# Performance work log

Measured on AMD Instinct MI355X. Metric: run time of the kernel, lower is better.

Reference implementation:

```python
import jax, jax.numpy as jnp
from jax import lax
import numpy as np

K = 256   # kernel_size == hidden channels (Haar basis size)
S = 16    # stride
BN_EPS = 1e-5


def _haar_matrix_unnorm(n):
    if n == 2:
        return np.array([[1.0, 1.0], [1.0, -1.0]])
    prev = _haar_matrix_unnorm(n // 2)
    top = np.kron(prev, np.array([1.0, 1.0]))
    bot = np.kron(np.eye(n // 2), np.array([1.0, -1.0]))
    return np.concatenate((top, bot))


def haar_matrix(n):
    h = _haar_matrix_unnorm(n)
    return h / np.linalg.norm(h, axis=1, keepdims=True)


def setup_inputs() -> dict:
    key = jax.random.key(0)
    ks = jax.random.split(key, 8)
    B, T = 64, 32768
    haar = jnp.asarray(haar_matrix(K), dtype=jnp.float32)          # [K, K]
    x = jax.random.normal(ks[0], (B, 1, T), dtype=jnp.float32)
    return {
        "x": x,
        # BitwiseConv1d(1, K, K, stride=S, padding=K)
        "conv_w": haar[:, None, :],                                 # [K, 1, K] (OIH)
        "conv_b": 0.01 * jax.random.normal(ks[1], (K,), dtype=jnp.float32),
        "conv_gate": jax.random.uniform(ks[2], (K, 1, K), dtype=jnp.float32),
        "conv_scale": jnp.ones((K,), dtype=jnp.float32),            # adaptive per-out-channel scale
        # BatchNorm1d(K)
        "bn_gamma": jnp.ones((K,), dtype=jnp.float32),
        "bn_beta": jnp.zeros((K,), dtype=jnp.float32),
        # BitwiseConvTranspose1d(K, 1, K, stride=S)
        "ct_w": haar.T[:, None, :],                                 # [K(in), 1(out), K] (IOH, torch layout)
        "ct_b": 0.01 * jax.random.normal(ks[3], (1,), dtype=jnp.float32),
        "ct_gate": jax.random.uniform(ks[4], (K, 1, K), dtype=jnp.float32),
        "ct_scale": jnp.ones((1,), dtype=jnp.float32),
    }


def _forward(x, conv_w, conv_b, conv_gate, conv_scale, bn_gamma, bn_beta,
             ct_w, ct_b, ct_gate, ct_scale):
    T = x.shape[2]
    # --- BitwiseConv1d: gated weights (in_bin/weight_bin = identity) ---
    # gate binarization maps gate -> (gate + 1) / 2, multiplied into weights
    w = conv_w * (conv_gate + 1.0) * 0.5                            # [K,1,K]
    h = lax.conv_general_dilated(
        x, w, window_strides=(S,), padding=[(K, K)],
        dimension_numbers=("NCH", "OIH", "NCH"))                  # [B,K,L]
    h = conv_scale[None, :, None] * (h + conv_b[None, :, None])    # adaptive scaling
    # --- ReLU then BatchNorm1d (training-mode batch statistics) ---
    h = jax.nn.relu(h)
    mu = jnp.mean(h, axis=(0, 2), keepdims=True)
    var = jnp.mean((h - mu) ** 2, axis=(0, 2), keepdims=True)
    h = (h - mu) * lax.rsqrt(var + BN_EPS)
    h = h * bn_gamma[None, :, None] + bn_beta[None, :, None]
    # --- BitwiseConvTranspose1d: gated weights, expressed as dilated conv ---
    wt = ct_w * (ct_gate + 1.0) * 0.5                               # [K_in, 1, K]
    # torch IOH -> regular-conv OIH with kernel flipped
    wr = jnp.flip(jnp.transpose(wt, (1, 0, 2)), axis=-1)            # [1, K, K]
    y = lax.conv_general_dilated(
        h, wr, window_strides=(1,), padding=[(K - 1, K - 1)],
        lhs_dilation=(S,), dimension_numbers=("NCH", "OIH", "NCH"))
    y = ct_scale[None, :, None] * (y + ct_b[None, :, None])
    # crop: out[:, :, K : T + K]
    return y[:, :, K:T + K]


def reference(x, conv_w, conv_b, conv_gate, conv_scale, bn_gamma, bn_beta,
              ct_w, ct_b, ct_gate, ct_scale):
    return _forward(x, conv_w, conv_b, conv_gate, conv_scale, bn_gamma, bn_beta,
                    ct_w, ct_b, ct_gate, ct_scale)
```

## Files before the change

kernel.cpp:

```cpp
#include <hip/hip_runtime.h>
#include <hip/hip_bf16.h>

#define BB 64
#define TT 32768
#define KK 256
#define LL 2065
#define NLT 9
#define NPART (BB*NLT)
#define NJ 19
#define HBSTR 72
#define NPT3 16
#define XG 2336

typedef __attribute__((ext_vector_type(8))) short short8;
typedef __attribute__((ext_vector_type(4))) float f32x4;
typedef __attribute__((ext_vector_type(4))) int int4v;
typedef __attribute__((ext_vector_type(2))) unsigned int uint2v;

__device__ __forceinline__ unsigned short f2bf(float f) {
    unsigned u = __builtin_bit_cast(unsigned, f);
    unsigned r = (u + 0x7FFFu + ((u >> 16) & 1u)) >> 16;
    return (unsigned short)r;
}
__device__ __forceinline__ unsigned pkbf(float a, float b) {
    unsigned r;
    asm("v_cvt_pk_bf16_f32 %0, %1, %2" : "=v"(r) : "v"(a), "v"(b));
    return r;
}
__device__ __forceinline__ void gload_lds16(const void* g, void* l) {
    __builtin_amdgcn_global_load_lds(
        (const __attribute__((address_space(1))) unsigned int*)g,
        (__attribute__((address_space(3))) unsigned int*)l, 16, 0, 0);
}

__global__ void k0x_xbf(const float* __restrict__ x, unsigned short* __restrict__ xbf)
{
    int idx = blockIdx.x*256 + threadIdx.x;
    int b = idx / XG, gi = idx - b*XG;
    unsigned short* dst = xbf + (size_t)idx*24;
    int4v w0, w1;
    if (gi < 16 || gi > 2063) {
        w0 = (int4v){0,0,0,0}; w1 = (int4v){0,0,0,0};
    } else {
        const float4* xv = (const float4*)(x + (size_t)b*TT + 16*(gi-16));
        float4 a0 = xv[0], a1 = xv[1], a2 = xv[2], a3 = xv[3];
        w0 = (int4v){ (int)pkbf(a0.x,a0.y), (int)pkbf(a0.z,a0.w),
                      (int)pkbf(a1.x,a1.y), (int)pkbf(a1.z,a1.w) };
        w1 = (int4v){ (int)pkbf(a2.x,a2.y), (int)pkbf(a2.z,a2.w),
                      (int)pkbf(a3.x,a3.y), (int)pkbf(a3.z,a3.w) };
    }
    *(int4v*)dst       = w0;
    *(int4v*)(dst + 8) = w1;
}

__global__ void k0_w1f(const float* __restrict__ cw, const float* __restrict__ cgt,
                       const float* __restrict__ cs, const float* __restrict__ cb,
                       unsigned short* __restrict__ W1f, float* __restrict__ cbs)
{
    int idx = blockIdx.x*256 + threadIdx.x;
    int lane = idx & 63, ntL = (idx>>6)&7, kk = (idx>>9)&7, half = idx>>12;
    int o = half*128 + ntL*16 + (lane&15);
    float sc = cs[o];
    int kbase = kk*32 + ((lane>>4)<<3);
    short8 v;
    #pragma unroll
    for (int i = 0; i < 8; ++i) {
        int gi = o*KK + kbase + i;
        v[i] = (short)f2bf(sc * cw[gi]*(cgt[gi]+1.0f)*0.5f);
    }
    *(short8*)(W1f + (size_t)idx*8) = v;
    if (blockIdx.x == 0) {
        int c = threadIdx.x;
        cbs[c] = cs[c]*cb[c];
    }
}

__global__ __launch_bounds__(256, 3)
void k1_conv(const unsigned short* __restrict__ xbf, const float* __restrict__ cbs,
             const unsigned short* __restrict__ W1f,
             unsigned short* __restrict__ hout,
             float* __restrict__ psum, float* __restrict__ psq)
{
    __shared__ __align__(16) char smem[13312 + 32768];
    char* xwinb = smem;
    char* wbuf  = smem + 13312;
    unsigned short* hb = (unsigned short*)smem;
    float* redS = (float*)(smem + 36864);
    float* redQ = (float*)(smem + 36864 + 4096);

    const int tid   = threadIdx.x;
    const int q     = blockIdx.x & 3;
    const int ltile = blockIdx.x >> 2;
    const int b     = blockIdx.y;
    const int l0    = ltile * 256;
    const int lane  = tid & 63;
    const int w     = tid >> 6;

    {
        #pragma unroll
        for (int it = 0; it < 8; ++it) {
            int ci = w*8 + it;
            int kk = ci >> 2, ntl = ci & 3;
            size_t so = (size_t)((((q>>1)*8 + kk)*8 + (q&1)*4 + ntl))*1024;
            gload_lds16((const char*)W1f + so + lane*16, wbuf + ci*1024);
        }
    }
    {
        const char* xsrc = (const char*)xbf + (size_t)b*(XG*48) + (size_t)ltile*12288;
        #pragma unroll
        for (int it = 0; it < 4; ++it) {
            int i = w + it*4;
            if (i < 13)
                gload_lds16(xsrc + i*1024 + lane*16, xwinb + i*1024);
        }
    }
    __syncthreads();

    f32x4 acc[4][4];
    #pragma unroll
    for (int mt = 0; mt < 4; ++mt)
        #pragma unroll
        for (int nt = 0; nt < 4; ++nt) acc[mt][nt] = (f32x4){0.f,0.f,0.f,0.f};

    const int gq = lane >> 4;
    const int Gt = 16*gq + 16*(gq>>1);
    const int abase = 48*((w<<6) + (lane & 15)) + Gt;

    #pragma unroll
    for (int kk = 0; kk < 8; ++kk) {
        short8 bfx[4], afw[4];
        #pragma unroll
        for (int nt = 0; nt < 4; ++nt)
            bfx[nt] = *(const short8*)(xwinb + abase + nt*768 + kk*96);
        #pragma unroll
        for (int mt = 0; mt < 4; ++mt)
            afw[mt] = *(const short8*)(wbuf + (kk*4 + mt)*1024 + lane*16);
        __builtin_amdgcn_s_setprio(1);
        #pragma unroll
        for (int mt = 0; mt < 4; ++mt)
            #pragma unroll
            for (int nt = 0; nt < 4; ++nt)
                acc[mt][nt] = __builtin_amdgcn_mfma_f32_16x16x32_bf16(afw[mt], bfx[nt], acc[mt][nt], 0, 0, 0);
        __builtin_amdgcn_s_setprio(0);
    }
    __syncthreads();

    const int c0 = q*64;
    const int g  = lane >> 4;
    const int li = lane & 15;
    #pragma unroll
    for (int mt = 0; mt < 4; ++mt) {
        int cq = c0 + mt*16 + g*4;
        f32x4 cbs4 = *(const f32x4*)&cbs[cq];
        f32x4 s4 = (f32x4){0.f,0.f,0.f,0.f};
        f32x4 q4 = (f32x4){0.f,0.f,0.f,0.f};
        #pragma unroll
        for (int nt = 0; nt < 4; ++nt) {
            int lloc = (w<<6) + nt*16 + li;
            f32x4 hv;
            #pragma unroll
            for (int rr = 0; rr < 4; ++rr)
                hv[rr] = fmaxf(acc[mt][nt][rr] + cbs4[rr], 0.0f);
            uint2v pkv = { pkbf(hv[0], hv[1]), pkbf(hv[2], hv[3]) };
            *(uint2v*)(hb + lloc*HBSTR + mt*16 + g*4) = pkv;
            if (l0 + lloc < LL) { s4 += hv; q4 += hv*hv; }
        }
        #pragma unroll
        for (int d = 1; d < 4; d <<= 1) {
            #pragma unroll
            for (int rr = 0; rr < 4; ++rr) {
                s4[rr] += __shfl_xor(s4[rr], d);
                q4[rr] += __shfl_xor(q4[rr], d);
            }
        }
        if ((li & 3) == 0) {
            int slot = ((w*4 + mt)*4 + g)*4 + (li >> 2);
            *(f32x4*)&redS[slot*4] = s4;
            *(f32x4*)&redQ[slot*4] = q4;
        }
    }
    __syncthreads();

    {
        const int rsub = tid >> 3;
        const int cpos = tid & 7;
        #pragma unroll
        for (int it = 0; it < 8; ++it) {
            int row = it*32 + rsub;
            int l = l0 + row;
            if (l < LL) {
                int4v v = *(const int4v*)(hb + row*HBSTR + cpos*8);
                *(int4v*)(hout + (((size_t)(b*LL + l)) << 8) + q*64 + cpos*8) = v;
            }
        }
    }
    if (tid < 64) {
        int mt = tid >> 4, gg = (tid >> 2) & 3, rr = tid & 3;
        float s = 0.f, qq = 0.f;
        #pragma unroll
        for (int wv = 0; wv < 4; ++wv)
            #pragma unroll
            for (int l4 = 0; l4 < 4; ++l4) {
                int slot = ((wv*4 + mt)*4 + gg)*4 + l4;
                s  += redS[slot*4 + rr];
                qq += redQ[slot*4 + rr];
            }
        int c = c0 + tid;
        int slot = b*NLT + ltile;
        psum[c*NPART + slot] = s;
        psq [c*NPART + slot] = qq;
    }
}

__global__ __launch_bounds__(256)
void k2_bn(const float* __restrict__ psum, const float* __restrict__ psq,
           const float* __restrict__ bng, const float* __restrict__ bnb,
           const float* __restrict__ ctw, const float* __restrict__ ctg,
           const float* __restrict__ ctscale,
           float* __restrict__ W3s, float* __restrict__ SWS)
{
    __shared__ double rs[4], rq[4];
    __shared__ float s_a, s_bc;
    __shared__ float swl[256];
    const int c = blockIdx.x;
    const int tid = threadIdx.x;
    double s = 0.0, q = 0.0;
    for (int i = tid; i < NPART; i += 256) {
        s += (double)psum[c*NPART + i];
        q += (double)psq [c*NPART + i];
    }
    for (int off = 32; off > 0; off >>= 1) {
        s += __shfl_down(s, off);
        q += __shfl_down(q, off);
    }
    if ((tid & 63) == 0) { rs[tid >> 6] = s; rq[tid >> 6] = q; }
    __syncthreads();
    if (tid == 0) {
        double st = rs[0]+rs[1]+rs[2]+rs[3];
        double qt = rq[0]+rq[1]+rq[2]+rq[3];
        const double cnt = (double)BB * (double)LL;
        double mu = st / cnt;
        double var = qt / cnt - mu*mu;
        float rsig = (float)(1.0 / sqrt(var + 1e-5));
        float a = bng[c] * rsig;
        s_a = a;
        s_bc = bnb[c] - (float)mu * a;
    }
    __syncthreads();
    float a = s_a, bc = s_bc, scl = ctscale[0];
    int gi = c*KK + tid;
    float wt = ctw[gi] * (ctg[gi] + 1.0f) * 0.5f;
    W3s[tid*KK + c] = scl * a * wt;
    swl[tid] = wt * bc;
    __syncthreads();
    if (tid < 16) {
        float acc2 = 0.0f;
        #pragma unroll
        for (int d = 0; d < 16; ++d) acc2 += swl[d*16 + tid];
        SWS[c*16 + tid] = acc2;
    }
}

__global__ __launch_bounds__(256)
void k2b_const(const float* __restrict__ SWS, const float* __restrict__ ctb,
               const float* __restrict__ ctscale, float* __restrict__ C2)
{
    __shared__ float accb[16][17];
    int tid = threadIdx.x;
    int r = tid & 15, cc = tid >> 4;
    float s = 0.0f;
    #pragma unroll
    for (int i = 0; i < 16; ++i) s += SWS[(cc*16 + i)*16 + r];
    accb[cc][r] = s;
    __syncthreads();
    if (tid < 16) {
        float t = 0.0f;
        #pragma unroll
        for (int i = 0; i < 16; ++i) t += accb[i][tid];
        C2[tid] = ctscale[0] * (t + ctb[0]);
    }
}

__global__ void k2c_b2f(const float* __restrict__ W3s, unsigned short* __restrict__ B2f)
{
    int idx = blockIdx.x*256 + threadIdx.x;
    int lane = idx & 63;
    int ntG  = (idx>>6) & 3;
    int kk   = (idx>>8) & 7;
    int j    = idx>>11;
    int c    = kk*32 + ((lane>>4)<<3);
    int r    = lane & 15;
    int d    = ntG + 15 - j;
    short8 v;
    if (d >= 0 && d <= 15) {
        const float* wr = W3s + (size_t)(16*d + r)*KK + c;
        #pragma unroll
        for (int i = 0; i < 8; ++i) v[i] = (short)f2bf(wr[i]);
    } else {
        #pragma unroll
        for (int i = 0; i < 8; ++i) v[i] = 0;
    }
    *(short8*)(B2f + (size_t)idx*8) = v;
}

__global__ __launch_bounds__(512, 4)
void k3_synth(const unsigned short* __restrict__ h, const unsigned short* __restrict__ B2f,
              const float* __restrict__ C2, float* __restrict__ out)
{
    __shared__ __align__(16) char As[144*512];
    const int tid  = threadIdx.x;
    const int lane = tid & 63;
    const int w    = tid >> 6;
    const int b    = blockIdx.y;
    const int P0   = blockIdx.x * 32;

    const char* hbase = (const char*)h + (((size_t)(b*LL) + 4*P0 + 1) << 9);

    {
        const int rl = lane >> 5;
        #pragma unroll
        for (int i = 0; i < 9; ++i) {
            int r0  = w*18 + i*2;
            int row = r0 + rl;
            int chunk = (lane & 31) ^ ((row >> 2) & 7);
            gload_lds16(hbase + (size_t)row*512 + chunk*16, As + r0*512);
        }
    }
    __syncthreads();

    const int li = lane & 15;
    const int gq = lane >> 4;

    f32x4 acc[2][4];
    #pragma unroll
    for (int mt = 0; mt < 2; ++mt)
        #pragma unroll
        for (int nt = 0; nt < 4; ++nt) acc[mt][nt] = (f32x4){0.f,0.f,0.f,0.f};

    #pragma unroll 1
    for (int jj = 0; jj < 3; ++jj) {
        const int j = w + jj*8;
        if (j >= NJ) break;
        short8 bfA[4], bfB[4];
        #pragma unroll
        for (int nt = 0; nt < 4; ++nt)
            if (nt >= j-15 && nt <= j)
                bfA[nt] = *(const short8*)(B2f + (((size_t)(j*8 + 0)*4 + nt)*64 + lane)*8);
        #pragma unroll
        for (int kk = 0; kk < 8; ++kk) {
            if (kk < 7) {
                #pragma unroll
                for (int nt = 0; nt < 4; ++nt)
                    if (nt >= j-15 && nt <= j)
                        bfB[nt] = *(const short8*)(B2f + (((size_t)(j*8 + kk+1)*4 + nt)*64 + lane)*8);
            }
            short8 af[2];
            #pragma unroll
            for (int mt = 0; mt < 2; ++mt) {
                int row = 64*mt + 4*li + j;
                int p = (kk*4 + gq) ^ ((row >> 2) & 7);
                af[mt] = *(const short8*)(As + row*512 + p*16);
            }
            __builtin_amdgcn_s_setprio(1);
            #pragma unroll
            for (int mt = 0; mt < 2; ++mt)
                #pragma unroll
                for (int nt = 0; nt < 4; ++nt)
                    if (nt >= j-15 && nt <= j)
                        acc[mt][nt] = __builtin_amdgcn_mfma_f32_16x16x32_bf16(af[mt], bfA[nt], acc[mt][nt], 0, 0, 0);
            __builtin_amdgcn_s_setprio(0);
            #pragma unroll
            for (int nt = 0; nt < 4; ++nt) bfA[nt] = bfB[nt];
        }
    }
    __syncthreads();

    float* red = (float*)As;
    #pragma unroll
    for (int mt = 0; mt < 2; ++mt)
        #pragma unroll
        for (int nt = 0; nt < 4; ++nt) {
            int u = nt*16 + li;
            #pragma unroll
            for (int rr = 0; rr < 4; ++rr) {
                int Pl = 16*mt + gq*4 + rr;
                red[w*2176 + Pl*68 + u] = acc[mt][nt][rr];
            }
        }
    __syncthreads();

    {
        int P = tid >> 4, uq = tid & 15;
        f32x4 s = (f32x4){0.f,0.f,0.f,0.f};
        #pragma unroll
        for (int c = 0; c < 8; ++c)
            s += *(const f32x4*)&red[c*2176 + P*68 + uq*4];
        int ub = (uq & 3)*4;
        f32x4 c2v = { C2[ub], C2[ub+1], C2[ub+2], C2[ub+3] };
        float* ob = out + (size_t)b*TT + (size_t)P0*64;
        *(f32x4*)&ob[P*64 + uq*4] = s + c2v;
    }
}

extern "C" void kernel_launch(void* const* d_in, const int* in_sizes, int n_in,
                              void* d_out, int out_size, void* d_ws, size_t ws_size,
                              hipStream_t stream)
{
    const float* x       = (const float*)d_in[0];
    const float* cw      = (const float*)d_in[1];
    const float* cb      = (const float*)d_in[2];
    const float* cgt     = (const float*)d_in[3];
    const float* cs      = (const float*)d_in[4];
    const float* bng     = (const float*)d_in[5];
    const float* bnb     = (const float*)d_in[6];
    const float* ctw     = (const float*)d_in[7];
    const float* ctb     = (const float*)d_in[8];
    const float* ctg     = (const float*)d_in[9];
    const float* ctscale = (const float*)d_in[10];
    float* out = (float*)d_out;

    char* ws = (char*)d_ws;
    size_t off = 0;
    unsigned short* h    = (unsigned short*)(ws + off); off += (size_t)BB*LL*KK*2;
    float* psum          = (float*)(ws + off);          off += (size_t)KK*NPART*4;
    float* psq           = (float*)(ws + off);          off += (size_t)KK*NPART*4;
    unsigned short* W1f  = (unsigned short*)(ws + off); off += 65536*2;
    float* W3s           = (float*)(ws + off);          off += (size_t)KK*KK*4;
    float* SWS           = (float*)(ws + off);          off += (size_t)KK*16*4;
    float* C2            = (float*)(ws + off);          off += 64;
    float* cbs           = (float*)(ws + off);          off += 1024;
    unsigned short* xbf  = (unsigned short*)(ws + off); off += (size_t)BB*XG*24*2;
    unsigned short* B2f  = (unsigned short*)(ws + off); off += (size_t)NJ*8*4*64*8*2;

    k0x_xbf <<<BB*XG/256, 256, 0, stream>>>(x, xbf);
    k0_w1f  <<<32, 256, 0, stream>>>(cw, cgt, cs, cb, W1f, cbs);
    k1_conv <<<dim3(36, BB), 256, 0, stream>>>(xbf, cbs, W1f, h, psum, psq);
    k2_bn   <<<KK, 256, 0, stream>>>(psum, psq, bng, bnb, ctw, ctg, ctscale, W3s, SWS);
    k2b_const<<<1, 256, 0, stream>>>(SWS, ctb, ctscale, C2);
    k2c_b2f <<<152, 256, 0, stream>>>(W3s, B2f);
    k3_synth<<<dim3(NPT3, BB), 512, 0, stream>>>(h, B2f, C2, out);
}
```

Before: 86.34 us.

## Retile conv and synthesis kernels: narrower conv channel tiles, wider synth tiles

The conv kernel now splits output channels into eight 32-channel slices instead of four 64-channel slices. That doubles the grid, halves the accumulators and LDS, and raises the occupancy hint to 5. The conv scale and bias are applied in the epilogue, removing the precomputed bias buffer. The synthesis kernel doubles its output tile to 64 positions per block with four M-tiles, drops the causal-band predicates, and lowers the occupancy hint to 1 with a larger LDS footprint. The conv now reads more redundant input windows and the synth runs fewer, larger blocks, which may reduce latency hiding.

```diff
diff --git a/kernel.cpp b/kernel.cpp
--- a/kernel.cpp
+++ b/kernel.cpp
@@ -8,9 +8,9 @@
 #define NLT 9
 #define NPART (BB*NLT)
 #define NJ 19
-#define HBSTR 72
-#define NPT3 16
+#define NPT3 8
 #define XG 2336
+#define HB8 36
 
 typedef __attribute__((ext_vector_type(8))) short short8;
 typedef __attribute__((ext_vector_type(4))) float f32x4;
@@ -54,43 +54,37 @@
 }
 
 __global__ void k0_w1f(const float* __restrict__ cw, const float* __restrict__ cgt,
-                       const float* __restrict__ cs, const float* __restrict__ cb,
-                       unsigned short* __restrict__ W1f, float* __restrict__ cbs)
+                       unsigned short* __restrict__ W1f)
 {
     int idx = blockIdx.x*256 + threadIdx.x;
     int lane = idx & 63, ntL = (idx>>6)&7, kk = (idx>>9)&7, half = idx>>12;
     int o = half*128 + ntL*16 + (lane&15);
-    float sc = cs[o];
     int kbase = kk*32 + ((lane>>4)<<3);
     short8 v;
     #pragma unroll
     for (int i = 0; i < 8; ++i) {
         int gi = o*KK + kbase + i;
-        v[i] = (short)f2bf(sc * cw[gi]*(cgt[gi]+1.0f)*0.5f);
+        v[i] = (short)f2bf(cw[gi]*(cgt[gi]+1.0f)*0.5f);
     }
     *(short8*)(W1f + (size_t)idx*8) = v;
-    if (blockIdx.x == 0) {
-        int c = threadIdx.x;
-        cbs[c] = cs[c]*cb[c];
-    }
-}
-
-__global__ __launch_bounds__(256, 3)
-void k1_conv(const unsigned short* __restrict__ xbf, const float* __restrict__ cbs,
-             const unsigned short* __restrict__ W1f,
+}
+
+__global__ __launch_bounds__(256, 5)
+void k1_conv(const unsigned short* __restrict__ xbf, const float* __restrict__ cs,
+             const float* __restrict__ cb, const unsigned short* __restrict__ W1f,
              unsigned short* __restrict__ hout,
              float* __restrict__ psum, float* __restrict__ psq)
 {
-    __shared__ __align__(16) char smem[13312 + 32768];
+    __shared__ __align__(16) char smem[13312 + 16384];
     char* xwinb = smem;
     char* wbuf  = smem + 13312;
     unsigned short* hb = (unsigned short*)smem;
-    float* redS = (float*)(smem + 36864);
-    float* redQ = (float*)(smem + 36864 + 4096);
+    float* redS = (float*)(smem + 18432);
+    float* redQ = (float*)(smem + 18432 + 512);
 
     const int tid   = threadIdx.x;
-    const int q     = blockIdx.x & 3;
-    const int ltile = blockIdx.x >> 2;
+    const int q8    = blockIdx.x & 7;
+    const int ltile = blockIdx.x >> 3;
     const int b     = blockIdx.y;
     const int l0    = ltile * 256;
     const int lane  = tid & 63;
@@ -98,10 +92,10 @@
 
     {
         #pragma unroll
-        for (int it = 0; it < 8; ++it) {
-            int ci = w*8 + it;
-            int kk = ci >> 2, ntl = ci & 3;
-            size_t so = (size_t)((((q>>1)*8 + kk)*8 + (q&1)*4 + ntl))*1024;
+        for (int it = 0; it < 4; ++it) {
+            int ci = w*4 + it;
+            int kk = ci >> 1, mt = ci & 1;
+            size_t so = (size_t)((((q8>>2)*8 + kk)*8 + (q8&3)*2 + mt))*1024;
             gload_lds16((const char*)W1f + so + lane*16, wbuf + ci*1024);
         }
     }
@@ -116,9 +110,9 @@
     }
     __syncthreads();
 
-    f32x4 acc[4][4];
-    #pragma unroll
-    for (int mt = 0; mt < 4; ++mt)
+    f32x4 acc[2][4];
+    #pragma unroll
+    for (int mt = 0; mt < 2; ++mt)
         #pragma unroll
         for (int nt = 0; nt < 4; ++nt) acc[mt][nt] = (f32x4){0.f,0.f,0.f,0.f};
 
@@ -128,16 +122,16 @@
 
     #pragma unroll
     for (int kk = 0; kk < 8; ++kk) {
-        short8 bfx[4], afw[4];
+        short8 bfx[4], afw[2];
         #pragma unroll
         for (int nt = 0; nt < 4; ++nt)
             bfx[nt] = *(const short8*)(xwinb + abase + nt*768 + kk*96);
         #pragma unroll
-        for (int mt = 0; mt < 4; ++mt)
-            afw[mt] = *(const short8*)(wbuf + (kk*4 + mt)*1024 + lane*16);
+        for (int mt = 0; mt < 2; ++mt)
+            afw[mt] = *(const short8*)(wbuf + (kk*2 + mt)*1024 + lane*16);
         __builtin_amdgcn_s_setprio(1);
         #pragma unroll
-        for (int mt = 0; mt < 4; ++mt)
+        for (int mt = 0; mt < 2; ++mt)
             #pragma unroll
             for (int nt = 0; nt < 4; ++nt)
                 acc[mt][nt] = __builtin_amdgcn_mfma_f32_16x16x32_bf16(afw[mt], bfx[nt], acc[mt][nt], 0, 0, 0);
@@ -145,13 +139,14 @@
     }
     __syncthreads();
 
-    const int c0 = q*64;
+    const int c0 = q8*32;
     const int g  = lane >> 4;
     const int li = lane & 15;
     #pragma unroll
-    for (int mt = 0; mt < 4; ++mt) {
+    for (int mt = 0; mt < 2; ++mt) {
         int cq = c0 + mt*16 + g*4;
-        f32x4 cbs4 = *(const f32x4*)&cbs[cq];
+        f32x4 cs4 = *(const f32x4*)&cs[cq];
+        f32x4 cb4 = *(const f32x4*)&cb[cq];
         f32x4 s4 = (f32x4){0.f,0.f,0.f,0.f};
         f32x4 q4 = (f32x4){0.f,0.f,0.f,0.f};
         #pragma unroll
@@ -160,51 +155,46 @@
             f32x4 hv;
             #pragma unroll
             for (int rr = 0; rr < 4; ++rr)
-                hv[rr] = fmaxf(acc[mt][nt][rr] + cbs4[rr], 0.0f);
+                hv[rr] = fmaxf(cs4[rr]*(acc[mt][nt][rr] + cb4[rr]), 0.0f);
             uint2v pkv = { pkbf(hv[0], hv[1]), pkbf(hv[2], hv[3]) };
-            *(uint2v*)(hb + lloc*HBSTR + mt*16 + g*4) = pkv;
+            *(uint2v*)(hb + lloc*HB8 + mt*16 + g*4) = pkv;
             if (l0 + lloc < LL) { s4 += hv; q4 += hv*hv; }
         }
         #pragma unroll
-        for (int d = 1; d < 4; d <<= 1) {
+        for (int d = 1; d < 16; d <<= 1) {
             #pragma unroll
             for (int rr = 0; rr < 4; ++rr) {
                 s4[rr] += __shfl_xor(s4[rr], d);
                 q4[rr] += __shfl_xor(q4[rr], d);
             }
         }
-        if ((li & 3) == 0) {
-            int slot = ((w*4 + mt)*4 + g)*4 + (li >> 2);
-            *(f32x4*)&redS[slot*4] = s4;
-            *(f32x4*)&redQ[slot*4] = q4;
+        if (li == 0) {
+            *(f32x4*)&redS[((w*2 + mt)*4 + g)*4] = s4;
+            *(f32x4*)&redQ[((w*2 + mt)*4 + g)*4] = q4;
         }
     }
     __syncthreads();
 
     {
-        const int rsub = tid >> 3;
-        const int cpos = tid & 7;
-        #pragma unroll
-        for (int it = 0; it < 8; ++it) {
-            int row = it*32 + rsub;
+        #pragma unroll
+        for (int it = 0; it < 4; ++it) {
+            int item = it*256 + tid;
+            int row = item >> 2, chunk = item & 3;
             int l = l0 + row;
             if (l < LL) {
-                int4v v = *(const int4v*)(hb + row*HBSTR + cpos*8);
-                *(int4v*)(hout + (((size_t)(b*LL + l)) << 8) + q*64 + cpos*8) = v;
+                int4v v = *(const int4v*)(hb + row*HB8 + chunk*8);
+                *(int4v*)(hout + (((size_t)(b*LL + l)) << 8) + q8*32 + chunk*8) = v;
             }
         }
     }
-    if (tid < 64) {
+    if (tid < 32) {
         int mt = tid >> 4, gg = (tid >> 2) & 3, rr = tid & 3;
         float s = 0.f, qq = 0.f;
         #pragma unroll
-        for (int wv = 0; wv < 4; ++wv)
-            #pragma unroll
-            for (int l4 = 0; l4 < 4; ++l4) {
-                int slot = ((wv*4 + mt)*4 + gg)*4 + l4;
-                s  += redS[slot*4 + rr];
-                qq += redQ[slot*4 + rr];
-            }
+        for (int wv = 0; wv < 4; ++wv) {
+            s  += redS[((wv*2 + mt)*4 + gg)*4 + rr];
+            qq += redQ[((wv*2 + mt)*4 + gg)*4 + rr];
+        }
         int c = c0 + tid;
         int slot = b*NLT + ltile;
         psum[c*NPART + slot] = s;
@@ -303,24 +293,24 @@
     *(short8*)(B2f + (size_t)idx*8) = v;
 }
 
-__global__ __launch_bounds__(512, 4)
+__global__ __launch_bounds__(512, 1)
 void k3_synth(const unsigned short* __restrict__ h, const unsigned short* __restrict__ B2f,
               const float* __restrict__ C2, float* __restrict__ out)
 {
-    __shared__ __align__(16) char As[144*512];
+    __shared__ __align__(16) char As[272*512];
     const int tid  = threadIdx.x;
     const int lane = tid & 63;
     const int w    = tid >> 6;
     const int b    = blockIdx.y;
-    const int P0   = blockIdx.x * 32;
+    const int P0   = blockIdx.x * 64;
 
     const char* hbase = (const char*)h + (((size_t)(b*LL) + 4*P0 + 1) << 9);
 
     {
         const int rl = lane >> 5;
         #pragma unroll
-        for (int i = 0; i < 9; ++i) {
-            int r0  = w*18 + i*2;
+        for (int i = 0; i < 17; ++i) {
+            int r0  = w*34 + i*2;
             int row = r0 + rl;
             int chunk = (lane & 31) ^ ((row >> 2) & 7);
             gload_lds16(hbase + (size_t)row*512 + chunk*16, As + r0*512);
@@ -331,9 +321,9 @@
     const int li = lane & 15;
     const int gq = lane >> 4;
 
-    f32x4 acc[2][4];
-    #pragma unroll
-    for (int mt = 0; mt < 2; ++mt)
+    f32x4 acc[4][4];
+    #pragma unroll
+    for (int mt = 0; mt < 4; ++mt)
         #pragma unroll
         for (int nt = 0; nt < 4; ++nt) acc[mt][nt] = (f32x4){0.f,0.f,0.f,0.f};
 
@@ -344,30 +334,27 @@
         short8 bfA[4], bfB[4];
         #pragma unroll
         for (int nt = 0; nt < 4; ++nt)
-            if (nt >= j-15 && nt <= j)
-                bfA[nt] = *(const short8*)(B2f + (((size_t)(j*8 + 0)*4 + nt)*64 + lane)*8);
+            bfA[nt] = *(const short8*)(B2f + (((size_t)(j*8 + 0)*4 + nt)*64 + lane)*8);
         #pragma unroll
         for (int kk = 0; kk < 8; ++kk) {
             if (kk < 7) {
                 #pragma unroll
                 for (int nt = 0; nt < 4; ++nt)
-                    if (nt >= j-15 && nt <= j)
-                        bfB[nt] = *(const short8*)(B2f + (((size_t)(j*8 + kk+1)*4 + nt)*64 + lane)*8);
+                    bfB[nt] = *(const short8*)(B2f + (((size_t)(j*8 + kk+1)*4 + nt)*64 + lane)*8);
             }
-            short8 af[2];
-            #pragma unroll
-            for (int mt = 0; mt < 2; ++mt) {
+            short8 af[4];
+            #pragma unroll
+            for (int mt = 0; mt < 4; ++mt) {
                 int row = 64*mt + 4*li + j;
                 int p = (kk*4 + gq) ^ ((row >> 2) & 7);
                 af[mt] = *(const short8*)(As + row*512 + p*16);
             }
             __builtin_amdgcn_s_setprio(1);
             #pragma unroll
-            for (int mt = 0; mt < 2; ++mt)
+            for (int mt = 0; mt < 4; ++mt)
                 #pragma unroll
                 for (int nt = 0; nt < 4; ++nt)
-                    if (nt >= j-15 && nt <= j)
-                        acc[mt][nt] = __builtin_amdgcn_mfma_f32_16x16x32_bf16(af[mt], bfA[nt], acc[mt][nt], 0, 0, 0);
+                    acc[mt][nt] = __builtin_amdgcn_mfma_f32_16x16x32_bf16(af[mt], bfA[nt], acc[mt][nt], 0, 0, 0);
             __builtin_amdgcn_s_setprio(0);
             #pragma unroll
             for (int nt = 0; nt < 4; ++nt) bfA[nt] = bfB[nt];
@@ -377,28 +364,32 @@
 
     float* red = (float*)As;
     #pragma unroll
-    for (int mt = 0; mt < 2; ++mt)
+    for (int mt = 0; mt < 4; ++mt)
         #pragma unroll
         for (int nt = 0; nt < 4; ++nt) {
             int u = nt*16 + li;
             #pragma unroll
             for (int rr = 0; rr < 4; ++rr) {
                 int Pl = 16*mt + gq*4 + rr;
-                red[w*2176 + Pl*68 + u] = acc[mt][nt][rr];
+                red[w*4352 + Pl*68 + u] = acc[mt][nt][rr];
             }
         }
     __syncthreads();
 
     {
-        int P = tid >> 4, uq = tid & 15;
-        f32x4 s = (f32x4){0.f,0.f,0.f,0.f};
-        #pragma unroll
-        for (int c = 0; c < 8; ++c)
-            s += *(const f32x4*)&red[c*2176 + P*68 + uq*4];
-        int ub = (uq & 3)*4;
-        f32x4 c2v = { C2[ub], C2[ub+1], C2[ub+2], C2[ub+3] };
         float* ob = out + (size_t)b*TT + (size_t)P0*64;
-        *(f32x4*)&ob[P*64 + uq*4] = s + c2v;
+        #pragma unroll
+        for (int it = 0; it < 2; ++it) {
+            int item = it*512 + tid;
+            int P = item >> 4, uq = item & 15;
+            f32x4 s = (f32x4){0.f,0.f,0.f,0.f};
+            #pragma unroll
+            for (int c = 0; c < 8; ++c)
+                s += *(const f32x4*)&red[c*4352 + P*68 + uq*4];
+            int ub = (uq & 3)*4;
+            f32x4 c2v = { C2[ub], C2[ub+1], C2[ub+2], C2[ub+3] };
+            *(f32x4*)&ob[P*64 + uq*4] = s + c2v;
+        }
     }
 }
 
@@ -428,13 +419,12 @@
     float* W3s           = (float*)(ws + off);          off += (size_t)KK*KK*4;
     float* SWS           = (float*)(ws + off);          off += (size_t)KK*16*4;
     float* C2            = (float*)(ws + off);          off += 64;
-    float* cbs           = (float*)(ws + off);          off += 1024;
     unsigned short* xbf  = (unsigned short*)(ws + off); off += (size_t)BB*XG*24*2;
     unsigned short* B2f  = (unsigned short*)(ws + off); off += (size_t)NJ*8*4*64*8*2;
 
     k0x_xbf <<<BB*XG/256, 256, 0, stream>>>(x, xbf);
-    k0_w1f  <<<32, 256, 0, stream>>>(cw, cgt, cs, cb, W1f, cbs);
-    k1_conv <<<dim3(36, BB), 256, 0, stream>>>(xbf, cbs, W1f, h, psum, psq);
+    k0_w1f  <<<32, 256, 0, stream>>>(cw, cgt, W1f);
+    k1_conv <<<dim3(72, BB), 256, 0, stream>>>(xbf, cs, cb, W1f, h, psum, psq);
     k2_bn   <<<KK, 256, 0, stream>>>(psum, psq, bng, bnb, ctw, ctg, ctscale, W3s, SWS);
     k2b_const<<<1, 256, 0, stream>>>(SWS, ctb, ctscale, C2);
     k2c_b2f <<<152, 256, 0, stream>>>(W3s, B2f);
```

Result: no change. 85.43 us (-1.0%).
